# Performance work log

Hardware: AMD Instinct MI355X
Metric: run time of the kernel (lower is better)

Reference implementation:

```python
import jax, jax.numpy as jnp
import numpy as np

B, H, W, C = 32, 56, 56, 192
WS, SHIFT, NH = 7, 3, 6
HD = C // NH
N = WS * WS
NW = (H // WS) * (W // WS)
SCALE = HD ** -0.5
EPS = 1e-5


def _relative_position_index():
    ch, cw = np.arange(WS), np.arange(WS)
    coords = np.stack(np.meshgrid(ch, cw, indexing='ij')).reshape(2, -1)  # [2, N]
    rel = coords[:, :, None] - coords[:, None, :]                          # [2, N, N]
    rel = rel.transpose(1, 2, 0)
    rel[:, :, 0] += WS - 1
    rel[:, :, 1] += WS - 1
    rel[:, :, 0] *= 2 * WS - 1
    return rel.sum(-1).astype(np.int32)  # [N, N]


def _shift_mask():
    # Standard Swin shifted-window attention mask, values in {0, -100}
    img = np.zeros((1, H, W, 1), dtype=np.float32)
    cnt = 0
    for hs in (slice(0, -WS), slice(-WS, -SHIFT), slice(-SHIFT, None)):
        for ws_ in (slice(0, -WS), slice(-WS, -SHIFT), slice(-SHIFT, None)):
            img[:, hs, ws_, :] = cnt
            cnt += 1
    w = img.reshape(1, H // WS, WS, W // WS, WS, 1).transpose(0, 1, 3, 2, 4, 5).reshape(-1, N)
    diff = w[:, None, :] - w[:, :, None]
    return np.where(diff != 0, -100.0, 0.0).astype(np.float32)  # [NW, N, N]


def setup_inputs() -> dict:
    key = jax.random.key(0)
    ks = jax.random.split(key, 8)
    inp = {
        'inputs': jax.random.normal(ks[0], (B, H * W, C), dtype=jnp.float32),
        'attention_mask': jnp.asarray(_shift_mask()),
        'norm1_g': jnp.ones((C,), jnp.float32),
        'norm1_b': jnp.zeros((C,), jnp.float32),
        'qkv_w': jax.random.normal(ks[1], (3 * C, C), jnp.float32) * 0.02,
        'qkv_b': jnp.zeros((3 * C,), jnp.float32),
        'rel_pos_table': jax.random.normal(ks[2], ((2 * WS - 1) ** 2, NH), jnp.float32) * 0.02,
        'rel_pos_index': jnp.asarray(_relative_position_index()),
        'proj_w': jax.random.normal(ks[3], (C, C), jnp.float32) * 0.02,
        'proj_b': jnp.zeros((C,), jnp.float32),
        'lin_w': jax.random.normal(ks[4], (C, C), jnp.float32) * 0.02,
        'lin_b': jnp.zeros((C,), jnp.float32),
    }
    return inp


def _layernorm(x, g, b):
    mu = x.mean(-1, keepdims=True)
    var = ((x - mu) ** 2).mean(-1, keepdims=True)
    return (x - mu) * jax.lax.rsqrt(var + EPS) * g + b


def reference(inputs, attention_mask, norm1_g, norm1_b, qkv_w, qkv_b,
              rel_pos_table, rel_pos_index, proj_w, proj_b, lin_w, lin_b):
    shortcut = inputs
    x = _layernorm(inputs, norm1_g, norm1_b).reshape(B, H, W, C)
    # cyclic shift (H,W divisible by WS -> no padding)
    x = jnp.roll(x, (-SHIFT, -SHIFT), axis=(1, 2))
    # window partition -> (B*NW, N, C)
    xw = x.reshape(B, H // WS, WS, W // WS, WS, C).transpose(0, 1, 3, 2, 4, 5)
    xw = xw.reshape(-1, N, C)
    B_ = xw.shape[0]
    # qkv
    qkv = xw @ qkv_w.T + qkv_b                          # [B_, N, 3C]
    qkv = qkv.reshape(B_, N, 3, NH, HD).transpose(2, 0, 3, 1, 4)
    q, k, v = qkv[0] * SCALE, qkv[1], qkv[2]            # [B_, NH, N, HD]
    scores = jnp.einsum('bhnd,bhmd->bhnm', q, k)        # [B_, NH, N, N]
    bias = rel_pos_table[rel_pos_index.reshape(-1)].reshape(N, N, NH).transpose(2, 0, 1)
    scores = scores + bias[None]
    # shift mask
    scores = scores.reshape(B, NW, NH, N, N) + attention_mask[None, :, None]
    probs = jax.nn.softmax(scores.reshape(B_, NH, N, N), axis=-1)
    ctx = jnp.einsum('bhnm,bhmd->bnhd', probs, v).reshape(B_, N, C)
    ctx = ctx @ proj_w.T + proj_b
    # window reverse
    x = ctx.reshape(B, H // WS, W // WS, WS, WS, C).transpose(0, 1, 3, 2, 4, 5).reshape(B, H, W, C)
    x = jnp.roll(x, (SHIFT, SHIFT), axis=(1, 2)).reshape(B, H * W, C)
    x = jax.nn.gelu(x @ lin_w.T + lin_b, approximate=False)
    return shortcut + x
```

## Files before the change

### kernel.cpp

```cpp
#include <hip/hip_runtime.h>
#include <hip/hip_bf16.h>
#include <math.h>

typedef __bf16 bf16_t;
typedef __attribute__((ext_vector_type(8))) __bf16 bf16x8;
typedef __attribute__((ext_vector_type(4))) float floatx4;

#define SCALE 0.17677669529663689f
#define MFMA __builtin_amdgcn_mfma_f32_16x16x32_bf16

__global__ __launch_bounds__(256)
void prep(const float* __restrict__ table, const int* __restrict__ rpi,
          const float* __restrict__ mask, const float* __restrict__ qkv_w,
          const float* __restrict__ lw, const float* __restrict__ pw,
          const float* __restrict__ pb, const float* __restrict__ lb,
          bf16_t* __restrict__ cb2, bf16_t* __restrict__ wcvt,
          bf16_t* __restrict__ wfo, float* __restrict__ bfb)
{
    const int blk = blockIdx.x, tid = threadIdx.x;
    if (blk < 6144) {
        int i = blk * 256 + tid;
        int idx = i & 15, lane = (i >> 4) & 63, mt = (i >> 10) & 3, wh = i >> 12;
        int win = wh / 6, h = wh - win * 6;
        int nt = idx >> 2, r = idx & 3;
        int m = mt * 16 + ((lane >> 4)) * 4 + r;
        int j = nt * 16 + (lane & 15);
        float v;
        if (j >= 49)      v = -1e30f;
        else if (m >= 49) v = 0.0f;
        else              v = table[rpi[m * 49 + j] * 6 + h] + mask[win * 2401 + m * 49 + j];
        cb2[i] = (bf16_t)v;
    } else if (blk < 6576) {
        int i = (blk - 6144) * 256 + tid;
        wcvt[i] = (bf16_t)qkv_w[i];
    } else {
        int o = blk - 6576, i = tid;
        if (i < 192) {
            float acc = 0.f;
            for (int c = 0; c < 192; ++c)
                acc += lw[o * 192 + c] * pw[c * 192 + i];
            wfo[o * 192 + i] = (bf16_t)acc;
            if (i == 0) {
                float b = lb[o];
                for (int c = 0; c < 192; ++c) b += lw[o * 192 + c] * pb[c];
                bfb[o] = b;
            }
        }
    }
}

__global__ __launch_bounds__(768, 3)
void fused_window(const float* __restrict__ inp, const float* __restrict__ g,
                  const float* __restrict__ bta, const bf16_t* __restrict__ wcvt,
                  const float* __restrict__ qkv_b, const bf16_t* __restrict__ cb2,
                  const bf16_t* __restrict__ wfo, const float* __restrict__ bfb,
                  float* __restrict__ out)
{
    __shared__ __align__(16) bf16_t lds[81040];
    const int tid = threadIdx.x;
    const int wv = tid >> 6;
    const int wwin = wv >= 6 ? 1 : 0;
    const int h = wv - wwin * 6;
    const int lane = tid & 63;
    const int quad = lane >> 4, lr = lane & 15;
    const int w = blockIdx.x * 2 + wwin;
    const int wh = (w & 63) * 6 + h;
    bf16_t* base = lds + wwin * 40520;
    bf16_t* XL = base;
    bf16_t* R  = base + 9800 + h * 5120;

    const int b = w >> 6, widx = w & 63;
    const int whh = widx >> 3, www = widx & 7;

    auto ldx = [&](int mt, int ks) -> bf16x8 {
        bf16x8 z = {};
        int row = mt * 16 + lr;
        if (row < 49) z = *(const bf16x8*)&XL[row * 200 + ks * 32 + quad * 8];
        return z;
    };

    {
        float g0 = g[lane], g1 = g[lane + 64], g2 = g[lane + 128];
        float b0 = bta[lane], b1 = bta[lane + 64], b2 = bta[lane + 128];
        for (int t = h; t < 49; t += 6) {
            int ii = t / 7, jj = t - ii * 7;
            int hh2 = whh * 7 + ii + 3; if (hh2 >= 56) hh2 -= 56;
            int ww2 = www * 7 + jj + 3; if (ww2 >= 56) ww2 -= 56;
            const float* row = inp + ((size_t)(b * 3136 + hh2 * 56 + ww2)) * 192;
            float v0 = row[lane], v1 = row[lane + 64], v2 = row[lane + 128];
            float s = v0 + v1 + v2;
            float sq = v0 * v0 + v1 * v1 + v2 * v2;
#pragma unroll
            for (int off = 32; off > 0; off >>= 1) {
                s  += __shfl_down(s, off);
                sq += __shfl_down(sq, off);
            }
            s = __shfl(s, 0); sq = __shfl(sq, 0);
            float mu  = s * (1.0f / 192.0f);
            float var = sq * (1.0f / 192.0f) - mu * mu;
            float inv = rsqrtf(var + 1e-5f);
            XL[t * 200 + lane]       = (bf16_t)((v0 - mu) * inv * g0 + b0);
            XL[t * 200 + lane + 64]  = (bf16_t)((v1 - mu) * inv * g1 + b1);
            XL[t * 200 + lane + 128] = (bf16_t)((v2 - mu) * inv * g2 + b2);
        }
    }
    __syncthreads();

    floatx4 acc[4][4];
#pragma unroll
    for (int mt = 0; mt < 4; ++mt)
#pragma unroll
        for (int nt = 0; nt < 4; ++nt) acc[mt][nt] = floatx4{0.f,0.f,0.f,0.f};

#pragma unroll
    for (int ks = 0; ks < 6; ++ks) {
        bf16x8 wf0 = *(const bf16x8*)(wcvt + (size_t)(h * 32 + lr) * 192 + ks * 32 + quad * 8);
        bf16x8 wf1 = *(const bf16x8*)(wcvt + (size_t)(h * 32 + 16 + lr) * 192 + ks * 32 + quad * 8);
        bf16x8 wf2 = *(const bf16x8*)(wcvt + (size_t)(192 + h * 32 + lr) * 192 + ks * 32 + quad * 8);
        bf16x8 wf3 = *(const bf16x8*)(wcvt + (size_t)(192 + h * 32 + 16 + lr) * 192 + ks * 32 + quad * 8);
#pragma unroll
        for (int mt = 0; mt < 4; ++mt) {
            bf16x8 xk = ldx(mt, ks);
            acc[mt][0] = MFMA(xk, wf0, acc[mt][0], 0, 0, 0);
            acc[mt][1] = MFMA(xk, wf1, acc[mt][1], 0, 0, 0);
            acc[mt][2] = MFMA(xk, wf2, acc[mt][2], 0, 0, 0);
            acc[mt][3] = MFMA(xk, wf3, acc[mt][3], 0, 0, 0);
        }
    }
    {
        float bq0 = qkv_b[h * 32 + lr],       bq1 = qkv_b[h * 32 + 16 + lr];
        float bk0 = qkv_b[192 + h * 32 + lr], bk1 = qkv_b[192 + h * 32 + 16 + lr];
#pragma unroll
        for (int mt = 0; mt < 4; ++mt)
#pragma unroll
            for (int r = 0; r < 4; ++r) {
                int tok = mt * 16 + quad * 4 + r;
                R[tok * 40 + lr]             = (bf16_t)((acc[mt][0][r] + bq0) * SCALE);
                R[tok * 40 + 16 + lr]        = (bf16_t)((acc[mt][1][r] + bq1) * SCALE);
                R[2560 + tok * 40 + lr]      = (bf16_t)(acc[mt][2][r] + bk0);
                R[2560 + tok * 40 + 16 + lr] = (bf16_t)(acc[mt][3][r] + bk1);
            }
    }

    bf16x8 qf[4], kf[4];
#pragma unroll
    for (int t = 0; t < 4; ++t) {
        qf[t] = *(const bf16x8*)&R[(t * 16 + lr) * 40 + quad * 8];
        kf[t] = *(const bf16x8*)&R[2560 + (t * 16 + lr) * 40 + quad * 8];
    }
    floatx4 s[4][4];
#pragma unroll
    for (int mt = 0; mt < 4; ++mt)
#pragma unroll
        for (int nt = 0; nt < 4; ++nt) s[mt][nt] = floatx4{0.f,0.f,0.f,0.f};
#pragma unroll
    for (int mt = 0; mt < 4; ++mt)
#pragma unroll
        for (int nt = 0; nt < 4; ++nt)
            s[mt][nt] = MFMA(qf[mt], kf[nt], s[mt][nt], 0, 0, 0);

    const bf16_t* cb = cb2 + (((size_t)wh * 4) * 64 + lane) * 16;
#pragma unroll
    for (int mt = 0; mt < 4; ++mt) {
        bf16x8 c0 = *(const bf16x8*)(cb + (size_t)mt * 1024);
        bf16x8 c1 = *(const bf16x8*)(cb + (size_t)mt * 1024 + 8);
#pragma unroll
        for (int r = 0; r < 4; ++r) {
            s[mt][0][r] += (float)c0[r];
            s[mt][1][r] += (float)c0[4 + r];
            s[mt][2][r] += (float)c1[r];
            s[mt][3][r] += (float)c1[4 + r];
        }
    }

#pragma unroll
    for (int mt = 0; mt < 4; ++mt) {
#pragma unroll
        for (int r = 0; r < 4; ++r) {
            float mx = fmaxf(fmaxf(s[mt][0][r], s[mt][1][r]),
                             fmaxf(s[mt][2][r], s[mt][3][r]));
#pragma unroll
            for (int off = 1; off < 16; off <<= 1)
                mx = fmaxf(mx, __shfl_xor(mx, off));
            float sum = 0.f;
#pragma unroll
            for (int nt = 0; nt < 4; ++nt) {
                float e = __expf(s[mt][nt][r] - mx);
                s[mt][nt][r] = e; sum += e;
            }
#pragma unroll
            for (int off = 1; off < 16; off <<= 1)
                sum += __shfl_xor(sum, off);
            float inv = 1.0f / sum;
#pragma unroll
            for (int nt = 0; nt < 4; ++nt) s[mt][nt][r] *= inv;
        }
    }

#pragma unroll
    for (int mt = 0; mt < 4; ++mt)
#pragma unroll
        for (int nt = 0; nt < 4; ++nt)
#pragma unroll
            for (int r = 0; r < 4; ++r)
                R[(mt * 16 + quad * 4 + r) * 72 + nt * 16 + lr] = (bf16_t)s[mt][nt][r];
    bf16x8 pf[4][2];
#pragma unroll
    for (int mt = 0; mt < 4; ++mt)
#pragma unroll
        for (int kt = 0; kt < 2; ++kt)
            pf[mt][kt] = *(const bf16x8*)&R[(mt * 16 + lr) * 72 + kt * 32 + quad * 8];

    floatx4 va[4][2];
#pragma unroll
    for (int mt = 0; mt < 4; ++mt) { va[mt][0] = floatx4{0.f,0.f,0.f,0.f}; va[mt][1] = floatx4{0.f,0.f,0.f,0.f}; }
#pragma unroll
    for (int ks = 0; ks < 6; ++ks) {
        bf16x8 wv0 = *(const bf16x8*)(wcvt + (size_t)(384 + h * 32 + lr) * 192 + ks * 32 + quad * 8);
        bf16x8 wv1 = *(const bf16x8*)(wcvt + (size_t)(384 + h * 32 + 16 + lr) * 192 + ks * 32 + quad * 8);
#pragma unroll
        for (int mt = 0; mt < 4; ++mt) {
            bf16x8 xk = ldx(mt, ks);
            va[mt][0] = MFMA(xk, wv0, va[mt][0], 0, 0, 0);
            va[mt][1] = MFMA(xk, wv1, va[mt][1], 0, 0, 0);
        }
    }
    {
        float bv0 = qkv_b[384 + h * 32 + lr], bv1 = qkv_b[384 + h * 32 + 16 + lr];
#pragma unroll
        for (int mt = 0; mt < 4; ++mt)
#pragma unroll
            for (int r = 0; r < 4; ++r) {
                int tok = mt * 16 + quad * 4 + r;
                R[lr * 72 + tok]        = (bf16_t)(va[mt][0][r] + bv0);
                R[(16 + lr) * 72 + tok] = (bf16_t)(va[mt][1][r] + bv1);
            }
    }

    bf16x8 vf[2][2];
#pragma unroll
    for (int nt = 0; nt < 2; ++nt)
#pragma unroll
        for (int kt = 0; kt < 2; ++kt)
            vf[nt][kt] = *(const bf16x8*)&R[(nt * 16 + lr) * 72 + kt * 32 + quad * 8];
    floatx4 c[4][2];
#pragma unroll
    for (int mt = 0; mt < 4; ++mt) { c[mt][0] = floatx4{0.f,0.f,0.f,0.f}; c[mt][1] = floatx4{0.f,0.f,0.f,0.f}; }
#pragma unroll
    for (int mt = 0; mt < 4; ++mt)
#pragma unroll
        for (int nt = 0; nt < 2; ++nt) {
            c[mt][nt] = MFMA(pf[mt][0], vf[nt][0], c[mt][nt], 0, 0, 0);
            c[mt][nt] = MFMA(pf[mt][1], vf[nt][1], c[mt][nt], 0, 0, 0);
        }
    __syncthreads();

#pragma unroll
    for (int mt = 0; mt < 4; ++mt)
#pragma unroll
        for (int nt = 0; nt < 2; ++nt)
#pragma unroll
            for (int r = 0; r < 4; ++r) {
                int tok = mt * 16 + quad * 4 + r;
                if (tok < 49)
                    XL[tok * 200 + h * 32 + nt * 16 + lr] = (bf16_t)c[mt][nt][r];
            }
    __syncthreads();

    floatx4 pr[4][2];
#pragma unroll
    for (int mt = 0; mt < 4; ++mt) { pr[mt][0] = floatx4{0.f,0.f,0.f,0.f}; pr[mt][1] = floatx4{0.f,0.f,0.f,0.f}; }
#pragma unroll
    for (int ks = 0; ks < 6; ++ks) {
        bf16x8 w0 = *(const bf16x8*)(wfo + (size_t)(h * 32 + lr) * 192 + ks * 32 + quad * 8);
        bf16x8 w1 = *(const bf16x8*)(wfo + (size_t)(h * 32 + 16 + lr) * 192 + ks * 32 + quad * 8);
#pragma unroll
        for (int mt = 0; mt < 4; ++mt) {
            bf16x8 af = ldx(mt, ks);
            pr[mt][0] = MFMA(af, w0, pr[mt][0], 0, 0, 0);
            pr[mt][1] = MFMA(af, w1, pr[mt][1], 0, 0, 0);
        }
    }
    {
        float pb0 = bfb[h * 32 + lr], pb1 = bfb[h * 32 + 16 + lr];
#pragma unroll
        for (int mt = 0; mt < 4; ++mt)
#pragma unroll
            for (int r = 0; r < 4; ++r) {
                int m = mt * 16 + quad * 4 + r;
                if (m < 49) {
                    int ii = m / 7, jj = m - ii * 7;
                    int hh2 = whh * 7 + ii + 3; if (hh2 >= 56) hh2 -= 56;
                    int ww2 = www * 7 + jj + 3; if (ww2 >= 56) ww2 -= 56;
                    size_t base2 = ((size_t)(b * 3136 + hh2 * 56 + ww2)) * 192 + h * 32;
                    float v0 = pr[mt][0][r] + pb0;
                    float v1 = pr[mt][1][r] + pb1;
                    float gx0 = 0.5f * v0 * (1.0f + erff(v0 * 0.70710678118654752f));
                    float gx1 = 0.5f * v1 * (1.0f + erff(v1 * 0.70710678118654752f));
                    out[base2 + lr]      = inp[base2 + lr]      + gx0;
                    out[base2 + 16 + lr] = inp[base2 + 16 + lr] + gx1;
                }
            }
    }
}

extern "C" void kernel_launch(void* const* d_in, const int* in_sizes, int n_in,
                              void* d_out, int out_size, void* d_ws, size_t ws_size,
                              hipStream_t stream)
{
    const float* inp    = (const float*)d_in[0];
    const float* mask   = (const float*)d_in[1];
    const float* g      = (const float*)d_in[2];
    const float* bta    = (const float*)d_in[3];
    const float* qkv_w  = (const float*)d_in[4];
    const float* qkv_b  = (const float*)d_in[5];
    const float* table  = (const float*)d_in[6];
    const int*   rpi    = (const int*)d_in[7];
    const float* proj_w = (const float*)d_in[8];
    const float* proj_b = (const float*)d_in[9];
    const float* lin_w  = (const float*)d_in[10];
    const float* lin_b  = (const float*)d_in[11];
    float* out = (float*)d_out;

    char* ws = (char*)d_ws;
    bf16_t* wcvt = (bf16_t*)(ws);
    bf16_t* wfo  = wcvt + 110592;
    float*  bfb  = (float*)(ws + 294912);
    bf16_t* cb2  = (bf16_t*)(ws + 300032);

    prep<<<6768, 256, 0, stream>>>(table, rpi, mask, qkv_w, lin_w, proj_w,
                                   proj_b, lin_b, cb2, wcvt, wfo, bfb);
    fused_window<<<1024, 768, 0, stream>>>(inp, g, bta, wcvt, qkv_b, cb2,
                                           wfo, bfb, out);
}
```

Baseline: 298.3 us.

## Merge prep and window kernels into one persistent cooperative kernel with grid sync

Replaces the separate prep launch and the fused window kernel with a single cooperative kernel of 256 blocks. Every block first does a grid-strided share of the bias/mask table, weight conversion and folded projection weights, then all blocks meet at a grid-wide barrier and loop persistently over window pairs. This removes one kernel launch and the gap between the two kernels, at the cost of a grid sync, only 256 resident blocks, and an extra __syncthreads per loop iteration.

```diff
diff --git a/kernel.cpp b/kernel.cpp
--- a/kernel.cpp
+++ b/kernel.cpp
@@ -1,4 +1,5 @@
 #include <hip/hip_runtime.h>
+#include <hip/hip_cooperative_groups.h>
 #include <hip/hip_bf16.h>
 #include <math.h>
 
@@ -9,68 +10,60 @@
 #define SCALE 0.17677669529663689f
 #define MFMA __builtin_amdgcn_mfma_f32_16x16x32_bf16
 
-__global__ __launch_bounds__(256)
-void prep(const float* __restrict__ table, const int* __restrict__ rpi,
-          const float* __restrict__ mask, const float* __restrict__ qkv_w,
-          const float* __restrict__ lw, const float* __restrict__ pw,
-          const float* __restrict__ pb, const float* __restrict__ lb,
+__global__ __launch_bounds__(768, 3)
+void mega(const float* __restrict__ inp, const float* __restrict__ g,
+          const float* __restrict__ bta, const float* __restrict__ qkv_w,
+          const float* __restrict__ qkv_b, const float* __restrict__ table,
+          const int* __restrict__ rpi, const float* __restrict__ mask,
+          const float* __restrict__ proj_w, const float* __restrict__ proj_b,
+          const float* __restrict__ lin_w, const float* __restrict__ lin_b,
           bf16_t* __restrict__ cb2, bf16_t* __restrict__ wcvt,
-          bf16_t* __restrict__ wfo, float* __restrict__ bfb)
+          bf16_t* __restrict__ wfo, float* __restrict__ bfb,
+          float* __restrict__ out)
 {
-    const int blk = blockIdx.x, tid = threadIdx.x;
-    if (blk < 6144) {
-        int i = blk * 256 + tid;
-        int idx = i & 15, lane = (i >> 4) & 63, mt = (i >> 10) & 3, wh = i >> 12;
-        int win = wh / 6, h = wh - win * 6;
+    __shared__ __align__(16) bf16_t lds[81040];
+    const int tid = threadIdx.x;
+    const int blk = blockIdx.x;
+    const int nthr = gridDim.x * 768;
+    const int gtid = blk * 768 + tid;
+
+    for (int i = gtid; i < 1572864; i += nthr) {
+        int idx = i & 15, lane = (i >> 4) & 63, mt = (i >> 10) & 3, whh_ = i >> 12;
+        int win = whh_ / 6, hh_ = whh_ - win * 6;
         int nt = idx >> 2, r = idx & 3;
         int m = mt * 16 + ((lane >> 4)) * 4 + r;
         int j = nt * 16 + (lane & 15);
         float v;
         if (j >= 49)      v = -1e30f;
         else if (m >= 49) v = 0.0f;
-        else              v = table[rpi[m * 49 + j] * 6 + h] + mask[win * 2401 + m * 49 + j];
+        else              v = table[rpi[m * 49 + j] * 6 + hh_] + mask[win * 2401 + m * 49 + j];
         cb2[i] = (bf16_t)v;
-    } else if (blk < 6576) {
-        int i = (blk - 6144) * 256 + tid;
+    }
+    for (int i = gtid; i < 110592; i += nthr)
         wcvt[i] = (bf16_t)qkv_w[i];
-    } else {
-        int o = blk - 6576, i = tid;
-        if (i < 192) {
-            float acc = 0.f;
-            for (int c = 0; c < 192; ++c)
-                acc += lw[o * 192 + c] * pw[c * 192 + i];
-            wfo[o * 192 + i] = (bf16_t)acc;
-            if (i == 0) {
-                float b = lb[o];
-                for (int c = 0; c < 192; ++c) b += lw[o * 192 + c] * pb[c];
-                bfb[o] = b;
-            }
-        }
+    for (int idx = gtid; idx < 36864; idx += nthr) {
+        int o = idx / 192, i = idx - o * 192;
+        float acc = 0.f;
+        for (int c = 0; c < 192; ++c)
+            acc += lin_w[o * 192 + c] * proj_w[c * 192 + i];
+        wfo[o * 192 + i] = (bf16_t)acc;
     }
-}
-
-__global__ __launch_bounds__(768, 3)
-void fused_window(const float* __restrict__ inp, const float* __restrict__ g,
-                  const float* __restrict__ bta, const bf16_t* __restrict__ wcvt,
-                  const float* __restrict__ qkv_b, const bf16_t* __restrict__ cb2,
-                  const bf16_t* __restrict__ wfo, const float* __restrict__ bfb,
-                  float* __restrict__ out)
-{
-    __shared__ __align__(16) bf16_t lds[81040];
-    const int tid = threadIdx.x;
+    for (int o = gtid; o < 192; o += nthr) {
+        float bb = lin_b[o];
+        for (int c = 0; c < 192; ++c) bb += lin_w[o * 192 + c] * proj_b[c];
+        bfb[o] = bb;
+    }
+    __threadfence();
+    cooperative_groups::this_grid().sync();
+
     const int wv = tid >> 6;
     const int wwin = wv >= 6 ? 1 : 0;
     const int h = wv - wwin * 6;
     const int lane = tid & 63;
     const int quad = lane >> 4, lr = lane & 15;
-    const int w = blockIdx.x * 2 + wwin;
-    const int wh = (w & 63) * 6 + h;
     bf16_t* base = lds + wwin * 40520;
     bf16_t* XL = base;
     bf16_t* R  = base + 9800 + h * 5120;
-
-    const int b = w >> 6, widx = w & 63;
-    const int whh = widx >> 3, www = widx & 7;
 
     auto ldx = [&](int mt, int ks) -> bf16x8 {
         bf16x8 z = {};
@@ -79,228 +72,236 @@
         return z;
     };
 
-    {
-        float g0 = g[lane], g1 = g[lane + 64], g2 = g[lane + 128];
-        float b0 = bta[lane], b1 = bta[lane + 64], b2 = bta[lane + 128];
-        for (int t = h; t < 49; t += 6) {
-            int ii = t / 7, jj = t - ii * 7;
-            int hh2 = whh * 7 + ii + 3; if (hh2 >= 56) hh2 -= 56;
-            int ww2 = www * 7 + jj + 3; if (ww2 >= 56) ww2 -= 56;
-            const float* row = inp + ((size_t)(b * 3136 + hh2 * 56 + ww2)) * 192;
-            float v0 = row[lane], v1 = row[lane + 64], v2 = row[lane + 128];
-            float s = v0 + v1 + v2;
-            float sq = v0 * v0 + v1 * v1 + v2 * v2;
-#pragma unroll
-            for (int off = 32; off > 0; off >>= 1) {
-                s  += __shfl_down(s, off);
-                sq += __shfl_down(sq, off);
-            }
-            s = __shfl(s, 0); sq = __shfl(sq, 0);
-            float mu  = s * (1.0f / 192.0f);
-            float var = sq * (1.0f / 192.0f) - mu * mu;
-            float inv = rsqrtf(var + 1e-5f);
-            XL[t * 200 + lane]       = (bf16_t)((v0 - mu) * inv * g0 + b0);
-            XL[t * 200 + lane + 64]  = (bf16_t)((v1 - mu) * inv * g1 + b1);
-            XL[t * 200 + lane + 128] = (bf16_t)((v2 - mu) * inv * g2 + b2);
-        }
-    }
-    __syncthreads();
-
-    floatx4 acc[4][4];
-#pragma unroll
-    for (int mt = 0; mt < 4; ++mt)
-#pragma unroll
-        for (int nt = 0; nt < 4; ++nt) acc[mt][nt] = floatx4{0.f,0.f,0.f,0.f};
-
-#pragma unroll
-    for (int ks = 0; ks < 6; ++ks) {
-        bf16x8 wf0 = *(const bf16x8*)(wcvt + (size_t)(h * 32 + lr) * 192 + ks * 32 + quad * 8);
-        bf16x8 wf1 = *(const bf16x8*)(wcvt + (size_t)(h * 32 + 16 + lr) * 192 + ks * 32 + quad * 8);
-        bf16x8 wf2 = *(const bf16x8*)(wcvt + (size_t)(192 + h * 32 + lr) * 192 + ks * 32 + quad * 8);
-        bf16x8 wf3 = *(const bf16x8*)(wcvt + (size_t)(192 + h * 32 + 16 + lr) * 192 + ks * 32 + quad * 8);
+    for (int p = blk; p < 1024; p += gridDim.x) {
+        const int w = p * 2 + wwin;
+        const int wh = (w & 63) * 6 + h;
+        const int b = w >> 6, widx = w & 63;
+        const int whh = widx >> 3, www = widx & 7;
+
+        {
+            float g0 = g[lane], g1 = g[lane + 64], g2 = g[lane + 128];
+            float b0 = bta[lane], b1 = bta[lane + 64], b2 = bta[lane + 128];
+            for (int t = h; t < 49; t += 6) {
+                int ii = t / 7, jj = t - ii * 7;
+                int hh2 = whh * 7 + ii + 3; if (hh2 >= 56) hh2 -= 56;
+                int ww2 = www * 7 + jj + 3; if (ww2 >= 56) ww2 -= 56;
+                const float* row = inp + ((size_t)(b * 3136 + hh2 * 56 + ww2)) * 192;
+                float v0 = row[lane], v1 = row[lane + 64], v2 = row[lane + 128];
+                float s = v0 + v1 + v2;
+                float sq = v0 * v0 + v1 * v1 + v2 * v2;
+#pragma unroll
+                for (int off = 32; off > 0; off >>= 1) {
+                    s  += __shfl_down(s, off);
+                    sq += __shfl_down(sq, off);
+                }
+                s = __shfl(s, 0); sq = __shfl(sq, 0);
+                float mu  = s * (1.0f / 192.0f);
+                float var = sq * (1.0f / 192.0f) - mu * mu;
+                float inv = rsqrtf(var + 1e-5f);
+                XL[t * 200 + lane]       = (bf16_t)((v0 - mu) * inv * g0 + b0);
+                XL[t * 200 + lane + 64]  = (bf16_t)((v1 - mu) * inv * g1 + b1);
+                XL[t * 200 + lane + 128] = (bf16_t)((v2 - mu) * inv * g2 + b2);
+            }
+        }
+        __syncthreads();
+
+        floatx4 acc[4][4];
+#pragma unroll
+        for (int mt = 0; mt < 4; ++mt)
+#pragma unroll
+            for (int nt = 0; nt < 4; ++nt) acc[mt][nt] = floatx4{0.f,0.f,0.f,0.f};
+
+#pragma unroll
+        for (int ks = 0; ks < 6; ++ks) {
+            bf16x8 wf0 = *(const bf16x8*)(wcvt + (size_t)(h * 32 + lr) * 192 + ks * 32 + quad * 8);
+            bf16x8 wf1 = *(const bf16x8*)(wcvt + (size_t)(h * 32 + 16 + lr) * 192 + ks * 32 + quad * 8);
+            bf16x8 wf2 = *(const bf16x8*)(wcvt + (size_t)(192 + h * 32 + lr) * 192 + ks * 32 + quad * 8);
+            bf16x8 wf3 = *(const bf16x8*)(wcvt + (size_t)(192 + h * 32 + 16 + lr) * 192 + ks * 32 + quad * 8);
+#pragma unroll
+            for (int mt = 0; mt < 4; ++mt) {
+                bf16x8 xk = ldx(mt, ks);
+                acc[mt][0] = MFMA(xk, wf0, acc[mt][0], 0, 0, 0);
+                acc[mt][1] = MFMA(xk, wf1, acc[mt][1], 0, 0, 0);
+                acc[mt][2] = MFMA(xk, wf2, acc[mt][2], 0, 0, 0);
+                acc[mt][3] = MFMA(xk, wf3, acc[mt][3], 0, 0, 0);
+            }
+        }
+        {
+            float bq0 = qkv_b[h * 32 + lr],       bq1 = qkv_b[h * 32 + 16 + lr];
+            float bk0 = qkv_b[192 + h * 32 + lr], bk1 = qkv_b[192 + h * 32 + 16 + lr];
+#pragma unroll
+            for (int mt = 0; mt < 4; ++mt)
+#pragma unroll
+                for (int r = 0; r < 4; ++r) {
+                    int tok = mt * 16 + quad * 4 + r;
+                    R[tok * 40 + lr]             = (bf16_t)((acc[mt][0][r] + bq0) * SCALE);
+                    R[tok * 40 + 16 + lr]        = (bf16_t)((acc[mt][1][r] + bq1) * SCALE);
+                    R[2560 + tok * 40 + lr]      = (bf16_t)(acc[mt][2][r] + bk0);
+                    R[2560 + tok * 40 + 16 + lr] = (bf16_t)(acc[mt][3][r] + bk1);
+                }
+        }
+
+        bf16x8 qf[4], kf[4];
+#pragma unroll
+        for (int t = 0; t < 4; ++t) {
+            qf[t] = *(const bf16x8*)&R[(t * 16 + lr) * 40 + quad * 8];
+            kf[t] = *(const bf16x8*)&R[2560 + (t * 16 + lr) * 40 + quad * 8];
+        }
+        floatx4 s[4][4];
+#pragma unroll
+        for (int mt = 0; mt < 4; ++mt)
+#pragma unroll
+            for (int nt = 0; nt < 4; ++nt) s[mt][nt] = floatx4{0.f,0.f,0.f,0.f};
+#pragma unroll
+        for (int mt = 0; mt < 4; ++mt)
+#pragma unroll
+            for (int nt = 0; nt < 4; ++nt)
+                s[mt][nt] = MFMA(qf[mt], kf[nt], s[mt][nt], 0, 0, 0);
+
+        const bf16_t* cb = cb2 + (((size_t)wh * 4) * 64 + lane) * 16;
 #pragma unroll
         for (int mt = 0; mt < 4; ++mt) {
-            bf16x8 xk = ldx(mt, ks);
-            acc[mt][0] = MFMA(xk, wf0, acc[mt][0], 0, 0, 0);
-            acc[mt][1] = MFMA(xk, wf1, acc[mt][1], 0, 0, 0);
-            acc[mt][2] = MFMA(xk, wf2, acc[mt][2], 0, 0, 0);
-            acc[mt][3] = MFMA(xk, wf3, acc[mt][3], 0, 0, 0);
-        }
-    }
-    {
-        float bq0 = qkv_b[h * 32 + lr],       bq1 = qkv_b[h * 32 + 16 + lr];
-        float bk0 = qkv_b[192 + h * 32 + lr], bk1 = qkv_b[192 + h * 32 + 16 + lr];
-#pragma unroll
-        for (int mt = 0; mt < 4; ++mt)
+            bf16x8 c0 = *(const bf16x8*)(cb + (size_t)mt * 1024);
+            bf16x8 c1 = *(const bf16x8*)(cb + (size_t)mt * 1024 + 8);
 #pragma unroll
             for (int r = 0; r < 4; ++r) {
-                int tok = mt * 16 + quad * 4 + r;
-                R[tok * 40 + lr]             = (bf16_t)((acc[mt][0][r] + bq0) * SCALE);
-                R[tok * 40 + 16 + lr]        = (bf16_t)((acc[mt][1][r] + bq1) * SCALE);
-                R[2560 + tok * 40 + lr]      = (bf16_t)(acc[mt][2][r] + bk0);
-                R[2560 + tok * 40 + 16 + lr] = (bf16_t)(acc[mt][3][r] + bk1);
-            }
-    }
-
-    bf16x8 qf[4], kf[4];
-#pragma unroll
-    for (int t = 0; t < 4; ++t) {
-        qf[t] = *(const bf16x8*)&R[(t * 16 + lr) * 40 + quad * 8];
-        kf[t] = *(const bf16x8*)&R[2560 + (t * 16 + lr) * 40 + quad * 8];
-    }
-    floatx4 s[4][4];
-#pragma unroll
-    for (int mt = 0; mt < 4; ++mt)
-#pragma unroll
-        for (int nt = 0; nt < 4; ++nt) s[mt][nt] = floatx4{0.f,0.f,0.f,0.f};
-#pragma unroll
-    for (int mt = 0; mt < 4; ++mt)
-#pragma unroll
-        for (int nt = 0; nt < 4; ++nt)
-            s[mt][nt] = MFMA(qf[mt], kf[nt], s[mt][nt], 0, 0, 0);
-
-    const bf16_t* cb = cb2 + (((size_t)wh * 4) * 64 + lane) * 16;
-#pragma unroll
-    for (int mt = 0; mt < 4; ++mt) {
-        bf16x8 c0 = *(const bf16x8*)(cb + (size_t)mt * 1024);
-        bf16x8 c1 = *(const bf16x8*)(cb + (size_t)mt * 1024 + 8);
-#pragma unroll
-        for (int r = 0; r < 4; ++r) {
-            s[mt][0][r] += (float)c0[r];
-            s[mt][1][r] += (float)c0[4 + r];
-            s[mt][2][r] += (float)c1[r];
-            s[mt][3][r] += (float)c1[4 + r];
-        }
-    }
-
-#pragma unroll
-    for (int mt = 0; mt < 4; ++mt) {
-#pragma unroll
-        for (int r = 0; r < 4; ++r) {
-            float mx = fmaxf(fmaxf(s[mt][0][r], s[mt][1][r]),
-                             fmaxf(s[mt][2][r], s[mt][3][r]));
-#pragma unroll
-            for (int off = 1; off < 16; off <<= 1)
-                mx = fmaxf(mx, __shfl_xor(mx, off));
-            float sum = 0.f;
-#pragma unroll
-            for (int nt = 0; nt < 4; ++nt) {
-                float e = __expf(s[mt][nt][r] - mx);
-                s[mt][nt][r] = e; sum += e;
-            }
-#pragma unroll
-            for (int off = 1; off < 16; off <<= 1)
-                sum += __shfl_xor(sum, off);
-            float inv = 1.0f / sum;
-#pragma unroll
-            for (int nt = 0; nt < 4; ++nt) s[mt][nt][r] *= inv;
-        }
-    }
-
-#pragma unroll
-    for (int mt = 0; mt < 4; ++mt)
-#pragma unroll
-        for (int nt = 0; nt < 4; ++nt)
-#pragma unroll
-            for (int r = 0; r < 4; ++r)
-                R[(mt * 16 + quad * 4 + r) * 72 + nt * 16 + lr] = (bf16_t)s[mt][nt][r];
-    bf16x8 pf[4][2];
-#pragma unroll
-    for (int mt = 0; mt < 4; ++mt)
-#pragma unroll
-        for (int kt = 0; kt < 2; ++kt)
-            pf[mt][kt] = *(const bf16x8*)&R[(mt * 16 + lr) * 72 + kt * 32 + quad * 8];
-
-    floatx4 va[4][2];
-#pragma unroll
-    for (int mt = 0; mt < 4; ++mt) { va[mt][0] = floatx4{0.f,0.f,0.f,0.f}; va[mt][1] = floatx4{0.f,0.f,0.f,0.f}; }
-#pragma unroll
-    for (int ks = 0; ks < 6; ++ks) {
-        bf16x8 wv0 = *(const bf16x8*)(wcvt + (size_t)(384 + h * 32 + lr) * 192 + ks * 32 + quad * 8);
-        bf16x8 wv1 = *(const bf16x8*)(wcvt + (size_t)(384 + h * 32 + 16 + lr) * 192 + ks * 32 + quad * 8);
+                s[mt][0][r] += (float)c0[r];
+                s[mt][1][r] += (float)c0[4 + r];
+                s[mt][2][r] += (float)c1[r];
+                s[mt][3][r] += (float)c1[4 + r];
+            }
+        }
+
 #pragma unroll
         for (int mt = 0; mt < 4; ++mt) {
-            bf16x8 xk = ldx(mt, ks);
-            va[mt][0] = MFMA(xk, wv0, va[mt][0], 0, 0, 0);
-            va[mt][1] = MFMA(xk, wv1, va[mt][1], 0, 0, 0);
-        }
-    }
-    {
-        float bv0 = qkv_b[384 + h * 32 + lr], bv1 = qkv_b[384 + h * 32 + 16 + lr];
-#pragma unroll
-        for (int mt = 0; mt < 4; ++mt)
 #pragma unroll
             for (int r = 0; r < 4; ++r) {
-                int tok = mt * 16 + quad * 4 + r;
-                R[lr * 72 + tok]        = (bf16_t)(va[mt][0][r] + bv0);
-                R[(16 + lr) * 72 + tok] = (bf16_t)(va[mt][1][r] + bv1);
-            }
-    }
-
-    bf16x8 vf[2][2];
-#pragma unroll
-    for (int nt = 0; nt < 2; ++nt)
-#pragma unroll
-        for (int kt = 0; kt < 2; ++kt)
-            vf[nt][kt] = *(const bf16x8*)&R[(nt * 16 + lr) * 72 + kt * 32 + quad * 8];
-    floatx4 c[4][2];
-#pragma unroll
-    for (int mt = 0; mt < 4; ++mt) { c[mt][0] = floatx4{0.f,0.f,0.f,0.f}; c[mt][1] = floatx4{0.f,0.f,0.f,0.f}; }
-#pragma unroll
-    for (int mt = 0; mt < 4; ++mt)
-#pragma unroll
-        for (int nt = 0; nt < 2; ++nt) {
-            c[mt][nt] = MFMA(pf[mt][0], vf[nt][0], c[mt][nt], 0, 0, 0);
-            c[mt][nt] = MFMA(pf[mt][1], vf[nt][1], c[mt][nt], 0, 0, 0);
-        }
-    __syncthreads();
-
-#pragma unroll
-    for (int mt = 0; mt < 4; ++mt)
+                float mx = fmaxf(fmaxf(s[mt][0][r], s[mt][1][r]),
+                                 fmaxf(s[mt][2][r], s[mt][3][r]));
+#pragma unroll
+                for (int off = 1; off < 16; off <<= 1)
+                    mx = fmaxf(mx, __shfl_xor(mx, off));
+                float sum = 0.f;
+#pragma unroll
+                for (int nt = 0; nt < 4; ++nt) {
+                    float e = __expf(s[mt][nt][r] - mx);
+                    s[mt][nt][r] = e; sum += e;
+                }
+#pragma unroll
+                for (int off = 1; off < 16; off <<= 1)
+                    sum += __shfl_xor(sum, off);
+                float inv = 1.0f / sum;
+#pragma unroll
+                for (int nt = 0; nt < 4; ++nt) s[mt][nt][r] *= inv;
+            }
+        }
+
+#pragma unroll
+        for (int mt = 0; mt < 4; ++mt)
+#pragma unroll
+            for (int nt = 0; nt < 4; ++nt)
+#pragma unroll
+                for (int r = 0; r < 4; ++r)
+                    R[(mt * 16 + quad * 4 + r) * 72 + nt * 16 + lr] = (bf16_t)s[mt][nt][r];
+        bf16x8 pf[4][2];
+#pragma unroll
+        for (int mt = 0; mt < 4; ++mt)
+#pragma unroll
+            for (int kt = 0; kt < 2; ++kt)
+                pf[mt][kt] = *(const bf16x8*)&R[(mt * 16 + lr) * 72 + kt * 32 + quad * 8];
+
+        floatx4 va[4][2];
+#pragma unroll
+        for (int mt = 0; mt < 4; ++mt) { va[mt][0] = floatx4{0.f,0.f,0.f,0.f}; va[mt][1] = floatx4{0.f,0.f,0.f,0.f}; }
+#pragma unroll
+        for (int ks = 0; ks < 6; ++ks) {
+            bf16x8 wv0 = *(const bf16x8*)(wcvt + (size_t)(384 + h * 32 + lr) * 192 + ks * 32 + quad * 8);
+            bf16x8 wv1 = *(const bf16x8*)(wcvt + (size_t)(384 + h * 32 + 16 + lr) * 192 + ks * 32 + quad * 8);
+#pragma unroll
+            for (int mt = 0; mt < 4; ++mt) {
+                bf16x8 xk = ldx(mt, ks);
+                va[mt][0] = MFMA(xk, wv0, va[mt][0], 0, 0, 0);
+                va[mt][1] = MFMA(xk, wv1, va[mt][1], 0, 0, 0);
+            }
+        }
+        {
+            float bv0 = qkv_b[384 + h * 32 + lr], bv1 = qkv_b[384 + h * 32 + 16 + lr];
+#pragma unroll
+            for (int mt = 0; mt < 4; ++mt)
+#pragma unroll
+                for (int r = 0; r < 4; ++r) {
+                    int tok = mt * 16 + quad * 4 + r;
+                    R[lr * 72 + tok]        = (bf16_t)(va[mt][0][r] + bv0);
+                    R[(16 + lr) * 72 + tok] = (bf16_t)(va[mt][1][r] + bv1);
+                }
+        }
+
+        bf16x8 vf[2][2];
 #pragma unroll
         for (int nt = 0; nt < 2; ++nt)
 #pragma unroll
-            for (int r = 0; r < 4; ++r) {
-                int tok = mt * 16 + quad * 4 + r;
-                if (tok < 49)
-                    XL[tok * 200 + h * 32 + nt * 16 + lr] = (bf16_t)c[mt][nt][r];
-            }
-    __syncthreads();
-
-    floatx4 pr[4][2];
-#pragma unroll
-    for (int mt = 0; mt < 4; ++mt) { pr[mt][0] = floatx4{0.f,0.f,0.f,0.f}; pr[mt][1] = floatx4{0.f,0.f,0.f,0.f}; }
-#pragma unroll
-    for (int ks = 0; ks < 6; ++ks) {
-        bf16x8 w0 = *(const bf16x8*)(wfo + (size_t)(h * 32 + lr) * 192 + ks * 32 + quad * 8);
-        bf16x8 w1 = *(const bf16x8*)(wfo + (size_t)(h * 32 + 16 + lr) * 192 + ks * 32 + quad * 8);
-#pragma unroll
-        for (int mt = 0; mt < 4; ++mt) {
-            bf16x8 af = ldx(mt, ks);
-            pr[mt][0] = MFMA(af, w0, pr[mt][0], 0, 0, 0);
-            pr[mt][1] = MFMA(af, w1, pr[mt][1], 0, 0, 0);
-        }
-    }
-    {
-        float pb0 = bfb[h * 32 + lr], pb1 = bfb[h * 32 + 16 + lr];
-#pragma unroll
-        for (int mt = 0; mt < 4; ++mt)
-#pragma unroll
-            for (int r = 0; r < 4; ++r) {
-                int m = mt * 16 + quad * 4 + r;
-                if (m < 49) {
-                    int ii = m / 7, jj = m - ii * 7;
-                    int hh2 = whh * 7 + ii + 3; if (hh2 >= 56) hh2 -= 56;
-                    int ww2 = www * 7 + jj + 3; if (ww2 >= 56) ww2 -= 56;
-                    size_t base2 = ((size_t)(b * 3136 + hh2 * 56 + ww2)) * 192 + h * 32;
-                    float v0 = pr[mt][0][r] + pb0;
-                    float v1 = pr[mt][1][r] + pb1;
-                    float gx0 = 0.5f * v0 * (1.0f + erff(v0 * 0.70710678118654752f));
-                    float gx1 = 0.5f * v1 * (1.0f + erff(v1 * 0.70710678118654752f));
-                    out[base2 + lr]      = inp[base2 + lr]      + gx0;
-                    out[base2 + 16 + lr] = inp[base2 + 16 + lr] + gx1;
-                }
-            }
+            for (int kt = 0; kt < 2; ++kt)
+                vf[nt][kt] = *(const bf16x8*)&R[(nt * 16 + lr) * 72 + kt * 32 + quad * 8];
+        floatx4 c[4][2];
+#pragma unroll
+        for (int mt = 0; mt < 4; ++mt) { c[mt][0] = floatx4{0.f,0.f,0.f,0.f}; c[mt][1] = floatx4{0.f,0.f,0.f,0.f}; }
+#pragma unroll
+        for (int mt = 0; mt < 4; ++mt)
+#pragma unroll
+            for (int nt = 0; nt < 2; ++nt) {
+                c[mt][nt] = MFMA(pf[mt][0], vf[nt][0], c[mt][nt], 0, 0, 0);
+                c[mt][nt] = MFMA(pf[mt][1], vf[nt][1], c[mt][nt], 0, 0, 0);
+            }
+        __syncthreads();
+
+#pragma unroll
+        for (int mt = 0; mt < 4; ++mt)
+#pragma unroll
+            for (int nt = 0; nt < 2; ++nt)
+#pragma unroll
+                for (int r = 0; r < 4; ++r) {
+                    int tok = mt * 16 + quad * 4 + r;
+                    if (tok < 49)
+                        XL[tok * 200 + h * 32 + nt * 16 + lr] = (bf16_t)c[mt][nt][r];
+                }
+        __syncthreads();
+
+        floatx4 pr[4][2];
+#pragma unroll
+        for (int mt = 0; mt < 4; ++mt) { pr[mt][0] = floatx4{0.f,0.f,0.f,0.f}; pr[mt][1] = floatx4{0.f,0.f,0.f,0.f}; }
+#pragma unroll
+        for (int ks = 0; ks < 6; ++ks) {
+            bf16x8 w0 = *(const bf16x8*)(wfo + (size_t)(h * 32 + lr) * 192 + ks * 32 + quad * 8);
+            bf16x8 w1 = *(const bf16x8*)(wfo + (size_t)(h * 32 + 16 + lr) * 192 + ks * 32 + quad * 8);
+#pragma unroll
+            for (int mt = 0; mt < 4; ++mt) {
+                bf16x8 af = ldx(mt, ks);
+                pr[mt][0] = MFMA(af, w0, pr[mt][0], 0, 0, 0);
+                pr[mt][1] = MFMA(af, w1, pr[mt][1], 0, 0, 0);
+            }
+        }
+        {
+            float pb0 = bfb[h * 32 + lr], pb1 = bfb[h * 32 + 16 + lr];
+#pragma unroll
+            for (int mt = 0; mt < 4; ++mt)
+#pragma unroll
+                for (int r = 0; r < 4; ++r) {
+                    int m = mt * 16 + quad * 4 + r;
+                    if (m < 49) {
+                        int ii = m / 7, jj = m - ii * 7;
+                        int hh2 = whh * 7 + ii + 3; if (hh2 >= 56) hh2 -= 56;
+                        int ww2 = www * 7 + jj + 3; if (ww2 >= 56) ww2 -= 56;
+                        size_t base2 = ((size_t)(b * 3136 + hh2 * 56 + ww2)) * 192 + h * 32;
+                        float v0 = pr[mt][0][r] + pb0;
+                        float v1 = pr[mt][1][r] + pb1;
+                        float gx0 = 0.5f * v0 * (1.0f + erff(v0 * 0.70710678118654752f));
+                        float gx1 = 0.5f * v1 * (1.0f + erff(v1 * 0.70710678118654752f));
+                        out[base2 + lr]      = inp[base2 + lr]      + gx0;
+                        out[base2 + 16 + lr] = inp[base2 + 16 + lr] + gx1;
+                    }
+                }
+        }
+        __syncthreads();
     }
 }
 
@@ -328,8 +329,11 @@
     float*  bfb  = (float*)(ws + 294912);
     bf16_t* cb2  = (bf16_t*)(ws + 300032);
 
-    prep<<<6768, 256, 0, stream>>>(table, rpi, mask, qkv_w, lin_w, proj_w,
-                                   proj_b, lin_b, cb2, wcvt, wfo, bfb);
-    fused_window<<<1024, 768, 0, stream>>>(inp, g, bta, wcvt, qkv_b, cb2,
-                                           wfo, bfb, out);
+    void* args[] = { (void*)&inp, (void*)&g, (void*)&bta, (void*)&qkv_w,
+                     (void*)&qkv_b, (void*)&table, (void*)&rpi, (void*)&mask,
+                     (void*)&proj_w, (void*)&proj_b, (void*)&lin_w, (void*)&lin_b,
+                     (void*)&cb2, (void*)&wcvt, (void*)&wfo, (void*)&bfb,
+                     (void*)&out };
+    hipLaunchCooperativeKernel((const void*)mega, dim3(256), dim3(768),
+                               (void**)args, 0, stream);
 }
```

Result: slower. 485.0 us (+62.6%).
